# Performance work log

Hardware: AMD Instinct MI355X
Metric: run time of the kernel (lower is better)

The kernel has to match this reference:

```python
import jax, jax.numpy as jnp
import numpy as np

DIM = 1024
HEADS = 16
DIM_HEAD = 64
INNER = HEADS * DIM_HEAD  # 1024
EPS = 1e-5


def layer_norm(x, g, b):
    mu = jnp.mean(x, axis=-1, keepdims=True)
    var = jnp.var(x, axis=-1, keepdims=True)
    return (x - mu) * jax.lax.rsqrt(var + EPS) * g + b


def setup_inputs() -> dict:
    key = jax.random.key(0)
    ks = jax.random.split(key, 8)
    s = 0.02
    return {
        "x": jax.random.normal(ks[0], (2, 2048, DIM), dtype=jnp.float32),
        "w_qkv": jax.random.normal(ks[1], (DIM, 3 * INNER), dtype=jnp.float32) * s,
        "w_out": jax.random.normal(ks[2], (INNER, DIM), dtype=jnp.float32) * s,
        "b_out": jnp.zeros((DIM,), jnp.float32),
        "g1": jnp.ones((DIM,), jnp.float32),
        "bt1": jnp.zeros((DIM,), jnp.float32),
        "g2": jnp.ones((DIM,), jnp.float32),
        "bt2": jnp.zeros((DIM,), jnp.float32),
        "w1": jax.random.normal(ks[3], (DIM, DIM), dtype=jnp.float32) * s,  # ff hidden = dim_out = DIM
        "b1": jnp.zeros((DIM,), jnp.float32),
        "w2": jax.random.normal(ks[4], (DIM, DIM), dtype=jnp.float32) * s,
        "b2": jnp.zeros((DIM,), jnp.float32),
    }


def reference(x, w_qkv, w_out, b_out, g1, bt1, g2, bt2, w1, b1, w2, b2):
    b, n, _ = x.shape
    scale = DIM_HEAD ** (-0.5)
    x_in = x
    xl = layer_norm(x, g1, bt1)
    qkv = xl @ w_qkv  # [b, n, 3*inner]
    q, k, v = jnp.split(qkv, 3, axis=-1)
    def split_heads(t):
        return t.reshape(b, n, HEADS, DIM_HEAD).transpose(0, 2, 1, 3)  # b h n d
    q, k, v = map(split_heads, (q, k, v))
    dots = jnp.einsum('bhid,bhjd->bhij', q, k) * scale
    attn = jax.nn.softmax(dots, axis=-1)
    out = jnp.einsum('bhij,bhjd->bhid', attn, v)
    out = out.transpose(0, 2, 1, 3).reshape(b, n, INNER)
    out = out @ w_out + b_out
    out = out + x_in
    h = layer_norm(out, g2, bt2)
    h = jax.nn.gelu(h @ w1 + b1, approximate=False) @ w2 + b2
    return h + out
```

## Files before the change

kernel.cpp:

```cpp
#include <hip/hip_runtime.h>
#include <math.h>

typedef __attribute__((ext_vector_type(4))) float f32x4;
typedef __attribute__((ext_vector_type(8))) short bf16x8;
typedef __attribute__((ext_vector_type(8))) unsigned short u16x8;

#define DIM 1024
#define SEQ 2048
#define NHEADS 16
#define DH 64

__device__ __forceinline__ unsigned short f2bf(float f) {
    unsigned int u = __builtin_bit_cast(unsigned int, f);
    u += 0x7fffu + ((u >> 16) & 1u);
    return (unsigned short)(u >> 16);
}

__device__ __forceinline__ unsigned int cvt_pk_bf16(float lo, float hi) {
    unsigned int r;
    asm("v_cvt_pk_bf16_f32 %0, %1, %2" : "=v"(r) : "v"(lo), "v"(hi));
    return r;
}

__device__ __forceinline__ float fexp2(float x) {
    float r;
    asm("v_exp_f32 %0, %1" : "=v"(r) : "v"(x));
    return r;
}

__device__ __forceinline__ void gld16(const unsigned short* g, unsigned short* l) {
    __builtin_amdgcn_global_load_lds((const __attribute__((address_space(1))) void*)g,
                                     (__attribute__((address_space(3))) void*)l, 16, 0, 0);
}

__global__ __launch_bounds__(256) void wtrans_all(const float* __restrict__ wq,
                                                  const float* __restrict__ wo,
                                                  const float* __restrict__ wf1,
                                                  const float* __restrict__ wf2,
                                                  unsigned short* __restrict__ oq,
                                                  unsigned short* __restrict__ oo,
                                                  unsigned short* __restrict__ of1,
                                                  unsigned short* __restrict__ of2, float sc) {
    int z = blockIdx.z;
    int bxi = blockIdx.x;
    if (z > 0 && bxi >= 32) return;
    const float* w = z == 0 ? wq : z == 1 ? wo : z == 2 ? wf1 : wf2;
    unsigned short* wt = z == 0 ? oq : z == 1 ? oo : z == 2 ? of1 : of2;
    int N = z == 0 ? 3072 : 1024;
    int scale_n = z == 0 ? 1024 : 0;
    const int K = 1024;
    __shared__ float t[32][33];
    int tid = threadIdx.x;
    int n0 = bxi * 32, k0 = blockIdx.y * 32;
    int c = tid & 31, rb = tid >> 5;
#pragma unroll
    for (int i = 0; i < 4; ++i) {
        int r = rb + i * 8;
        t[r][c] = w[(size_t)(k0 + r) * N + n0 + c];
    }
    __syncthreads();
#pragma unroll
    for (int i = 0; i < 4; ++i) {
        int r = rb + i * 8;
        float v = t[c][r];
        if (n0 + r < scale_n) v *= sc;
        wt[(size_t)(n0 + r) * K + k0 + c] = f2bf(v);
    }
}

__global__ __launch_bounds__(256) void ln_kernel(const float* __restrict__ x,
                                                 const float* __restrict__ g,
                                                 const float* __restrict__ bt,
                                                 unsigned short* __restrict__ o) {
    int row = blockIdx.x, tid = threadIdx.x;
    const float4* xr = (const float4*)(x + (size_t)row * DIM);
    float4 v = xr[tid];
    float s1 = v.x + v.y + v.z + v.w;
    float s2 = v.x * v.x + v.y * v.y + v.z * v.z + v.w * v.w;
#pragma unroll
    for (int m = 32; m >= 1; m >>= 1) {
        s1 += __shfl_xor(s1, m);
        s2 += __shfl_xor(s2, m);
    }
    __shared__ float r1[4], r2[4];
    int w = tid >> 6;
    if ((tid & 63) == 0) { r1[w] = s1; r2[w] = s2; }
    __syncthreads();
    s1 = r1[0] + r1[1] + r1[2] + r1[3];
    s2 = r2[0] + r2[1] + r2[2] + r2[3];
    float mu = s1 * (1.0f / DIM);
    float var = s2 * (1.0f / DIM) - mu * mu;
    float rstd = rsqrtf(var + 1e-5f);
    float4 g4 = ((const float4*)g)[tid];
    float4 b4 = ((const float4*)bt)[tid];
    ushort4 ov;
    ov.x = f2bf((v.x - mu) * rstd * g4.x + b4.x);
    ov.y = f2bf((v.y - mu) * rstd * g4.y + b4.y);
    ov.z = f2bf((v.z - mu) * rstd * g4.z + b4.z);
    ov.w = f2bf((v.w - mu) * rstd * g4.w + b4.w);
    *(ushort4*)(o + (size_t)row * DIM + tid * 4) = ov;
}

template <int BN, int BK, int OBF, int BIAS, int GELU_, int RESID>
__global__ __launch_bounds__(256) void gemm_kernel(const unsigned short* __restrict__ A,
                                                   const unsigned short* __restrict__ BT,
                                                   void* __restrict__ C,
                                                   const float* __restrict__ bias,
                                                   const float* __restrict__ resid,
                                                   int M, int N, int K, int nbx) {
    constexpr int U = BK / 8;
    constexpr int NAU = 128 * U;
    constexpr int NBU = BN * U;
    constexpr int PT = (NAU + NBU) / 256;
    constexpr int NJ = BN / 32;
    constexpr int KK = BK / 32;
    __shared__ unsigned short As[3][128 * BK];
    __shared__ unsigned short Bs[3][BN * BK];
    int tid = threadIdx.x;
    int lane = tid & 63, w = tid >> 6;
    int l15 = lane & 15, lhi = lane >> 4;
    int nwg = gridDim.x, wg = blockIdx.x;
    int swz = (wg & 7) * (nwg >> 3) + (wg >> 3);
    int bx = swz % nbx, by = swz / nbx;
    int row0 = by * 128, col0 = bx * BN;
    int wrow = (w >> 1) * 64, wcol = (w & 1) * (16 * NJ);
    f32x4 zero = {0.f, 0.f, 0.f, 0.f};
    f32x4 acc[4][NJ];
#pragma unroll
    for (int i = 0; i < 4; ++i)
#pragma unroll
        for (int j = 0; j < NJ; ++j) acc[i][j] = zero;
    auto stage = [&](int buf, int kt) {
#pragma unroll
        for (int p = 0; p < PT; ++p) {
            if (p * 256 < NAU) {
                int u = tid + p * 256;
                int r = u / U, cu = u % U;
                int scu = cu ^ (r & (U - 1));
                gld16(A + (size_t)(row0 + r) * K + kt * BK + scu * 8, &As[buf][0] + u * 8);
            } else {
                int ub = tid + p * 256 - NAU;
                int r = ub / U, cu = ub % U;
                int scu = cu ^ (r & (U - 1));
                gld16(BT + (size_t)(col0 + r) * K + kt * BK + scu * 8, &Bs[buf][0] + ub * 8);
            }
        }
    };
    int nk = K / BK;
    stage(0, 0);
    stage(1, 1);
    asm volatile("s_waitcnt vmcnt(%0)" ::"i"(PT) : "memory");
    __builtin_amdgcn_s_barrier();
    __builtin_amdgcn_sched_barrier(0);
    int cur = 0;
    for (int kt = 0; kt < nk; ++kt) {
        int nxt2 = cur + 2 >= 3 ? cur - 1 : cur + 2;
        if (kt + 2 < nk) stage(nxt2, kt + 2);
        const unsigned short* Ab = &As[cur][0];
        const unsigned short* Bb = &Bs[cur][0];
        bf16x8 af[4][KK], bfr[NJ][KK];
#pragma unroll
        for (int i = 0; i < 4; ++i)
#pragma unroll
            for (int kk = 0; kk < KK; ++kk) {
                int rr = wrow + i * 16 + l15;
                int up = (kk * 4 + lhi) ^ (rr & (U - 1));
                af[i][kk] = *(const bf16x8*)&Ab[rr * BK + up * 8];
            }
#pragma unroll
        for (int j = 0; j < NJ; ++j)
#pragma unroll
            for (int kk = 0; kk < KK; ++kk) {
                int rr = wcol + j * 16 + l15;
                int up = (kk * 4 + lhi) ^ (rr & (U - 1));
                bfr[j][kk] = *(const bf16x8*)&Bb[rr * BK + up * 8];
            }
#pragma unroll
        for (int kk = 0; kk < KK; ++kk)
#pragma unroll
            for (int i = 0; i < 4; ++i)
#pragma unroll
                for (int j = 0; j < NJ; ++j)
                    acc[i][j] = __builtin_amdgcn_mfma_f32_16x16x32_bf16(af[i][kk], bfr[j][kk],
                                                                        acc[i][j], 0, 0, 0);
        __builtin_amdgcn_sched_barrier(0);
        if (kt + 1 < nk) {
            if (kt + 2 < nk)
                asm volatile("s_waitcnt vmcnt(%0)" ::"i"(PT) : "memory");
            else
                asm volatile("s_waitcnt vmcnt(0)" ::: "memory");
            __builtin_amdgcn_s_barrier();
            __builtin_amdgcn_sched_barrier(0);
        }
        cur = cur + 1 == 3 ? 0 : cur + 1;
    }
#pragma unroll
    for (int i = 0; i < 4; ++i)
#pragma unroll
        for (int j = 0; j < NJ; ++j)
#pragma unroll
            for (int r = 0; r < 4; ++r) {
                int row = row0 + wrow + i * 16 + lhi * 4 + r;
                int col = col0 + wcol + j * 16 + l15;
                float v = acc[i][j][r];
                if (BIAS) v += bias[col];
                if (GELU_) v = 0.5f * v * (1.0f + erff(v * 0.70710678118f));
                if (RESID) v += resid[(size_t)row * N + col];
                if (OBF)
                    ((unsigned short*)C)[(size_t)row * N + col] = f2bf(v);
                else
                    ((float*)C)[(size_t)row * N + col] = v;
            }
}

__global__ __launch_bounds__(256) void vtrans_kernel(const unsigned short* __restrict__ qkv,
                                                     unsigned short* __restrict__ vt) {
    __shared__ unsigned short t[64 * 72];
    int tid = threadIdx.x;
    int nt = blockIdx.x & 31, h = (blockIdx.x >> 5) & 15, b = blockIdx.x >> 9;
#pragma unroll
    for (int p = 0; p < 2; ++p) {
        int c = tid + p * 256;
        int n = c >> 3, s = (c & 7) * 8;
        *(uint4*)&t[n * 72 + s] =
            *(const uint4*)(qkv + (size_t)(b * SEQ + nt * 64 + n) * 3072 + 2048 + h * 64 + s);
    }
    __syncthreads();
#pragma unroll
    for (int p = 0; p < 2; ++p) {
        int c = tid + p * 256;
        int d = c >> 3, s0 = (c & 7) * 8;
        u16x8 val;
#pragma unroll
        for (int j = 0; j < 8; ++j) {
            int s = s0 + j;
            int sig = (s & 32) | ((s & 4) << 2) | ((s & 24) >> 1) | (s & 3);
            val[j] = t[sig * 72 + d];
        }
        *(u16x8*)(vt + ((size_t)(b * NHEADS + h) * DH + d) * SEQ + nt * 64 + s0) = val;
    }
}

__global__ __launch_bounds__(256) void attn_kernel(const unsigned short* __restrict__ qkv,
                                                   const unsigned short* __restrict__ vt,
                                                   unsigned short* __restrict__ o) {
    __shared__ unsigned short Ks[2][64 * 64];
    __shared__ unsigned short Vs[2][64 * 64];
    int tid = threadIdx.x;
    int lane = tid & 63, w = tid >> 6;
    int l15 = lane & 15, lhi = lane >> 4;
    int wg = blockIdx.x;
    int swz = (wg & 7) * 128 + (wg >> 3);
    int qt = swz & 31, h = (swz >> 5) & 15, b = swz >> 9;
    const unsigned short* qb =
        qkv + (size_t)(b * SEQ + qt * 64 + w * 16 + l15) * 3072 + h * DH;
    bf16x8 qf0 = *(const bf16x8*)(qb + lhi * 8);
    bf16x8 qf1 = *(const bf16x8*)(qb + 32 + lhi * 8);
    f32x4 zero = {0.f, 0.f, 0.f, 0.f};
    f32x4 oacc[4], lacc = zero;
#pragma unroll
    for (int i = 0; i < 4; ++i) oacc[i] = zero;
    const short one_s = (short)0x3F80;
    bf16x8 ones = {one_s, one_s, one_s, one_s, one_s, one_s, one_s, one_s};
    int srow = tid >> 3;
    int scx = (tid & 7) ^ (srow & 7);
    const unsigned short* kb = qkv + (size_t)b * SEQ * 3072 + 1024 + h * DH;
    const unsigned short* vb = vt + (size_t)(b * NHEADS + h) * DH * SEQ;
    const unsigned short* k0 = kb + (size_t)srow * 3072 + scx * 8;
    const unsigned short* v0 = vb + (size_t)srow * SEQ + scx * 8;
    auto stage = [&](int buf, int kt) {
        unsigned short* lk = &Ks[buf][0] + tid * 8;
        unsigned short* lv = &Vs[buf][0] + tid * 8;
        gld16(k0 + (size_t)kt * 64 * 3072, lk);
        gld16(k0 + ((size_t)kt * 64 + 32) * 3072, lk + 2048);
        gld16(v0 + kt * 64, lv);
        gld16(v0 + (size_t)32 * SEQ + kt * 64, lv + 2048);
    };
    const int NT = SEQ / 64;
    stage(0, 0);
    asm volatile("s_waitcnt vmcnt(0)" ::: "memory");
    __builtin_amdgcn_s_barrier();
    __builtin_amdgcn_sched_barrier(0);
    int kx = l15 & 7;
    for (int kt = 0; kt < NT; ++kt) {
        int cur = kt & 1;
        if (kt + 1 < NT) stage(cur ^ 1, kt + 1);
        const unsigned short* Kc = &Ks[cur][0];
        const unsigned short* Vc = &Vs[cur][0];
        f32x4 sacc[4];
#pragma unroll
        for (int nt = 0; nt < 4; ++nt) {
            bf16x8 kf0 = *(const bf16x8*)&Kc[(nt * 16 + l15) * 64 + ((lhi ^ kx) * 8)];
            bf16x8 kf1 = *(const bf16x8*)&Kc[(nt * 16 + l15) * 64 + (((4 + lhi) ^ kx) * 8)];
            f32x4 z = __builtin_amdgcn_mfma_f32_16x16x32_bf16(kf0, qf0, zero, 0, 0, 0);
            sacc[nt] = __builtin_amdgcn_mfma_f32_16x16x32_bf16(kf1, qf1, z, 0, 0, 0);
        }
        bf16x8 pf[2];
#pragma unroll
        for (int kc = 0; kc < 2; ++kc) {
            union { bf16x8 v; unsigned int u[4]; } pu;
            pu.u[0] = cvt_pk_bf16(fexp2(sacc[2 * kc][0]), fexp2(sacc[2 * kc][1]));
            pu.u[1] = cvt_pk_bf16(fexp2(sacc[2 * kc][2]), fexp2(sacc[2 * kc][3]));
            pu.u[2] = cvt_pk_bf16(fexp2(sacc[2 * kc + 1][0]), fexp2(sacc[2 * kc + 1][1]));
            pu.u[3] = cvt_pk_bf16(fexp2(sacc[2 * kc + 1][2]), fexp2(sacc[2 * kc + 1][3]));
            pf[kc] = pu.v;
        }
#pragma unroll
        for (int dt = 0; dt < 4; ++dt)
#pragma unroll
            for (int kc = 0; kc < 2; ++kc) {
                bf16x8 vf = *(const bf16x8*)&Vc[(dt * 16 + l15) * 64 + (((kc * 4 + lhi) ^ kx) * 8)];
                oacc[dt] = __builtin_amdgcn_mfma_f32_16x16x32_bf16(vf, pf[kc], oacc[dt], 0, 0, 0);
            }
        lacc = __builtin_amdgcn_mfma_f32_16x16x32_bf16(ones, pf[0], lacc, 0, 0, 0);
        lacc = __builtin_amdgcn_mfma_f32_16x16x32_bf16(ones, pf[1], lacc, 0, 0, 0);
        __builtin_amdgcn_sched_barrier(0);
        if (kt + 1 < NT) {
            asm volatile("s_waitcnt vmcnt(0)" ::: "memory");
            __builtin_amdgcn_s_barrier();
            __builtin_amdgcn_sched_barrier(0);
        }
    }
    float rl = 1.0f / lacc[0];
    size_t orow = (size_t)(b * SEQ + qt * 64 + w * 16 + l15) * DIM + h * DH;
#pragma unroll
    for (int dt = 0; dt < 4; ++dt) {
        ushort4 st;
        st.x = f2bf(oacc[dt][0] * rl);
        st.y = f2bf(oacc[dt][1] * rl);
        st.z = f2bf(oacc[dt][2] * rl);
        st.w = f2bf(oacc[dt][3] * rl);
        *(ushort4*)(o + orow + dt * 16 + lhi * 4) = st;
    }
}

extern "C" void kernel_launch(void* const* d_in, const int* in_sizes, int n_in,
                              void* d_out, int out_size, void* d_ws, size_t ws_size,
                              hipStream_t stream) {
    (void)in_sizes; (void)n_in; (void)out_size; (void)ws_size;
    const float* x = (const float*)d_in[0];
    const float* w_qkv = (const float*)d_in[1];
    const float* w_out = (const float*)d_in[2];
    const float* b_out = (const float*)d_in[3];
    const float* g1 = (const float*)d_in[4];
    const float* bt1 = (const float*)d_in[5];
    const float* g2 = (const float*)d_in[6];
    const float* bt2 = (const float*)d_in[7];
    const float* w1 = (const float*)d_in[8];
    const float* b1 = (const float*)d_in[9];
    const float* w2 = (const float*)d_in[10];
    const float* b2 = (const float*)d_in[11];
    float* out = (float*)d_out;

    char* ws = (char*)d_ws;
    size_t off = 0;
    auto alloc = [&](size_t bytes) {
        void* p = ws + off;
        off += (bytes + 255) & ~(size_t)255;
        return p;
    };
    const int R = 2 * SEQ;
    unsigned short* xl    = (unsigned short*)alloc((size_t)R * DIM * 2);
    unsigned short* wqkvT = (unsigned short*)alloc((size_t)3 * DIM * DIM * 2);
    unsigned short* woutT = (unsigned short*)alloc((size_t)DIM * DIM * 2);
    unsigned short* w1T   = (unsigned short*)alloc((size_t)DIM * DIM * 2);
    unsigned short* w2T   = (unsigned short*)alloc((size_t)DIM * DIM * 2);
    unsigned short* qkvb  = (unsigned short*)alloc((size_t)R * 3 * DIM * 2);
    unsigned short* vtb   = (unsigned short*)alloc((size_t)R * DIM * 2);
    unsigned short* attO  = (unsigned short*)alloc((size_t)R * DIM * 2);
    unsigned short* h2    = (unsigned short*)alloc((size_t)R * DIM * 2);
    unsigned short* ffn1  = (unsigned short*)alloc((size_t)R * DIM * 2);

    const float CS = 0.125f * 1.44269504f;
    wtrans_all<<<dim3(96, 32, 4), 256, 0, stream>>>(w_qkv, w_out, w1, w2, wqkvT, woutT, w1T, w2T, CS);

    ln_kernel<<<R, 256, 0, stream>>>(x, g1, bt1, xl);
    gemm_kernel<128, 32, 1, 0, 0, 0><<<dim3((3 * DIM / 128) * (R / 128)), 256, 0, stream>>>(
        xl, wqkvT, qkvb, nullptr, nullptr, R, 3 * DIM, DIM, 3 * DIM / 128);
    vtrans_kernel<<<2 * NHEADS * (SEQ / 64), 256, 0, stream>>>(qkvb, vtb);
    attn_kernel<<<2 * NHEADS * (SEQ / 64), 256, 0, stream>>>(qkvb, vtb, attO);
    gemm_kernel<64, 64, 0, 1, 0, 1><<<dim3((DIM / 64) * (R / 128)), 256, 0, stream>>>(
        attO, woutT, out, b_out, x, R, DIM, DIM, DIM / 64);
    ln_kernel<<<R, 256, 0, stream>>>(out, g2, bt2, h2);
    gemm_kernel<64, 64, 1, 1, 1, 0><<<dim3((DIM / 64) * (R / 128)), 256, 0, stream>>>(
        h2, w1T, ffn1, b1, nullptr, R, DIM, DIM, DIM / 64);
    gemm_kernel<64, 64, 0, 1, 0, 1><<<dim3((DIM / 64) * (R / 128)), 256, 0, stream>>>(
        ffn1, w2T, out, b2, out, R, DIM, DIM, DIM / 64);
}
```

Before: 168.4 us.

## Split attention over two KV halves and combine partials in a new kernel

```diff
diff --git a/kernel.cpp b/kernel.cpp
--- a/kernel.cpp
+++ b/kernel.cpp
@@ -243,15 +243,16 @@
 
 __global__ __launch_bounds__(256) void attn_kernel(const unsigned short* __restrict__ qkv,
                                                    const unsigned short* __restrict__ vt,
-                                                   unsigned short* __restrict__ o) {
-    __shared__ unsigned short Ks[2][64 * 64];
-    __shared__ unsigned short Vs[2][64 * 64];
+                                                   float* __restrict__ po,
+                                                   float* __restrict__ pl) {
+    __shared__ unsigned short Ks[64 * 64];
+    __shared__ unsigned short Vs[64 * 64];
     int tid = threadIdx.x;
     int lane = tid & 63, w = tid >> 6;
     int l15 = lane & 15, lhi = lane >> 4;
     int wg = blockIdx.x;
-    int swz = (wg & 7) * 128 + (wg >> 3);
-    int qt = swz & 31, h = (swz >> 5) & 15, b = swz >> 9;
+    int swz = (wg & 7) * 256 + (wg >> 3);
+    int qt = swz & 31, half = (swz >> 5) & 1, h = (swz >> 6) & 15, b = swz >> 10;
     const unsigned short* qb =
         qkv + (size_t)(b * SEQ + qt * 64 + w * 16 + l15) * 3072 + h * DH;
     bf16x8 qf0 = *(const bf16x8*)(qb + lhi * 8);
@@ -268,30 +269,26 @@
     const unsigned short* vb = vt + (size_t)(b * NHEADS + h) * DH * SEQ;
     const unsigned short* k0 = kb + (size_t)srow * 3072 + scx * 8;
     const unsigned short* v0 = vb + (size_t)srow * SEQ + scx * 8;
-    auto stage = [&](int buf, int kt) {
-        unsigned short* lk = &Ks[buf][0] + tid * 8;
-        unsigned short* lv = &Vs[buf][0] + tid * 8;
-        gld16(k0 + (size_t)kt * 64 * 3072, lk);
-        gld16(k0 + ((size_t)kt * 64 + 32) * 3072, lk + 2048);
-        gld16(v0 + kt * 64, lv);
-        gld16(v0 + (size_t)32 * SEQ + kt * 64, lv + 2048);
+    auto stage = [&](int kg) {
+        unsigned short* lk = &Ks[0] + tid * 8;
+        unsigned short* lv = &Vs[0] + tid * 8;
+        gld16(k0 + (size_t)kg * 64 * 3072, lk);
+        gld16(k0 + ((size_t)kg * 64 + 32) * 3072, lk + 2048);
+        gld16(v0 + kg * 64, lv);
+        gld16(v0 + (size_t)32 * SEQ + kg * 64, lv + 2048);
     };
-    const int NT = SEQ / 64;
-    stage(0, 0);
-    asm volatile("s_waitcnt vmcnt(0)" ::: "memory");
-    __builtin_amdgcn_s_barrier();
-    __builtin_amdgcn_sched_barrier(0);
     int kx = l15 & 7;
-    for (int kt = 0; kt < NT; ++kt) {
-        int cur = kt & 1;
-        if (kt + 1 < NT) stage(cur ^ 1, kt + 1);
-        const unsigned short* Kc = &Ks[cur][0];
-        const unsigned short* Vc = &Vs[cur][0];
+    const int NT2 = SEQ / 64 / 2;
+    for (int kt = 0; kt < NT2; ++kt) {
+        stage(half * NT2 + kt);
+        asm volatile("s_waitcnt vmcnt(0)" ::: "memory");
+        __builtin_amdgcn_s_barrier();
+        __builtin_amdgcn_sched_barrier(0);
         f32x4 sacc[4];
 #pragma unroll
         for (int nt = 0; nt < 4; ++nt) {
-            bf16x8 kf0 = *(const bf16x8*)&Kc[(nt * 16 + l15) * 64 + ((lhi ^ kx) * 8)];
-            bf16x8 kf1 = *(const bf16x8*)&Kc[(nt * 16 + l15) * 64 + (((4 + lhi) ^ kx) * 8)];
+            bf16x8 kf0 = *(const bf16x8*)&Ks[(nt * 16 + l15) * 64 + ((lhi ^ kx) * 8)];
+            bf16x8 kf1 = *(const bf16x8*)&Ks[(nt * 16 + l15) * 64 + (((4 + lhi) ^ kx) * 8)];
             f32x4 z = __builtin_amdgcn_mfma_f32_16x16x32_bf16(kf0, qf0, zero, 0, 0, 0);
             sacc[nt] = __builtin_amdgcn_mfma_f32_16x16x32_bf16(kf1, qf1, z, 0, 0, 0);
         }
@@ -309,29 +306,41 @@
         for (int dt = 0; dt < 4; ++dt)
 #pragma unroll
             for (int kc = 0; kc < 2; ++kc) {
-                bf16x8 vf = *(const bf16x8*)&Vc[(dt * 16 + l15) * 64 + (((kc * 4 + lhi) ^ kx) * 8)];
+                bf16x8 vf = *(const bf16x8*)&Vs[(dt * 16 + l15) * 64 + (((kc * 4 + lhi) ^ kx) * 8)];
                 oacc[dt] = __builtin_amdgcn_mfma_f32_16x16x32_bf16(vf, pf[kc], oacc[dt], 0, 0, 0);
             }
         lacc = __builtin_amdgcn_mfma_f32_16x16x32_bf16(ones, pf[0], lacc, 0, 0, 0);
         lacc = __builtin_amdgcn_mfma_f32_16x16x32_bf16(ones, pf[1], lacc, 0, 0, 0);
         __builtin_amdgcn_sched_barrier(0);
-        if (kt + 1 < NT) {
-            asm volatile("s_waitcnt vmcnt(0)" ::: "memory");
+        if (kt + 1 < NT2) {
             __builtin_amdgcn_s_barrier();
             __builtin_amdgcn_sched_barrier(0);
         }
     }
-    float rl = 1.0f / lacc[0];
-    size_t orow = (size_t)(b * SEQ + qt * 64 + w * 16 + l15) * DIM + h * DH;
+    int rrow = b * SEQ + qt * 64 + w * 16 + l15;
+    float* pob = po + ((size_t)half * 4096 + rrow) * DIM + h * DH;
 #pragma unroll
     for (int dt = 0; dt < 4; ++dt) {
-        ushort4 st;
-        st.x = f2bf(oacc[dt][0] * rl);
-        st.y = f2bf(oacc[dt][1] * rl);
-        st.z = f2bf(oacc[dt][2] * rl);
-        st.w = f2bf(oacc[dt][3] * rl);
-        *(ushort4*)(o + orow + dt * 16 + lhi * 4) = st;
-    }
+        float4 st = {oacc[dt][0], oacc[dt][1], oacc[dt][2], oacc[dt][3]};
+        *(float4*)(pob + dt * 16 + lhi * 4) = st;
+    }
+    if (lhi == 0) pl[((size_t)half * 4096 + rrow) * NHEADS + h] = lacc[0];
+}
+
+__global__ __launch_bounds__(256) void attn_combine(const float* __restrict__ po,
+                                                    const float* __restrict__ pl,
+                                                    unsigned short* __restrict__ o) {
+    int r = blockIdx.x, tid = threadIdx.x;
+    int d0 = tid * 4, h = d0 >> 6;
+    float4 a = *(const float4*)(po + (size_t)r * DIM + d0);
+    float4 c = *(const float4*)(po + (size_t)(4096 + r) * DIM + d0);
+    float rl = 1.0f / (pl[(size_t)r * NHEADS + h] + pl[(size_t)(4096 + r) * NHEADS + h]);
+    ushort4 ov;
+    ov.x = f2bf((a.x + c.x) * rl);
+    ov.y = f2bf((a.y + c.y) * rl);
+    ov.z = f2bf((a.z + c.z) * rl);
+    ov.w = f2bf((a.w + c.w) * rl);
+    *(ushort4*)(o + (size_t)r * DIM + d0) = ov;
 }
 
 extern "C" void kernel_launch(void* const* d_in, const int* in_sizes, int n_in,
@@ -370,6 +379,8 @@
     unsigned short* attO  = (unsigned short*)alloc((size_t)R * DIM * 2);
     unsigned short* h2    = (unsigned short*)alloc((size_t)R * DIM * 2);
     unsigned short* ffn1  = (unsigned short*)alloc((size_t)R * DIM * 2);
+    float* po = (float*)alloc((size_t)2 * R * DIM * 4);
+    float* pl = (float*)alloc((size_t)2 * R * NHEADS * 4);
 
     const float CS = 0.125f * 1.44269504f;
     wtrans_all<<<dim3(96, 32, 4), 256, 0, stream>>>(w_qkv, w_out, w1, w2, wqkvT, woutT, w1T, w2T, CS);
@@ -378,7 +389,8 @@
     gemm_kernel<128, 32, 1, 0, 0, 0><<<dim3((3 * DIM / 128) * (R / 128)), 256, 0, stream>>>(
         xl, wqkvT, qkvb, nullptr, nullptr, R, 3 * DIM, DIM, 3 * DIM / 128);
     vtrans_kernel<<<2 * NHEADS * (SEQ / 64), 256, 0, stream>>>(qkvb, vtb);
-    attn_kernel<<<2 * NHEADS * (SEQ / 64), 256, 0, stream>>>(qkvb, vtb, attO);
+    attn_kernel<<<2 * NHEADS * (SEQ / 64) * 2, 256, 0, stream>>>(qkvb, vtb, po, pl);
+    attn_combine<<<R, 256, 0, stream>>>(po, pl, attO);
     gemm_kernel<64, 64, 0, 1, 0, 1><<<dim3((DIM / 64) * (R / 128)), 256, 0, stream>>>(
         attO, woutT, out, b_out, x, R, DIM, DIM, DIM / 64);
     ln_kernel<<<R, 256, 0, stream>>>(out, g2, bt2, h2);
```

Result: slower. 178.8 us (+6.2%).

## Fuse LN1 into weight transpose, V-transpose into QKV GEMM, store residual in bf16

Applied to the files above, without the earlier changes.

```diff
diff --git a/kernel.cpp b/kernel.cpp
--- a/kernel.cpp
+++ b/kernel.cpp
@@ -16,6 +16,11 @@
     return (unsigned short)(u >> 16);
 }
 
+__device__ __forceinline__ float bf2f(unsigned short s) {
+    unsigned int u = (unsigned int)s << 16;
+    return __builtin_bit_cast(float, u);
+}
+
 __device__ __forceinline__ unsigned int cvt_pk_bf16(float lo, float hi) {
     unsigned int r;
     asm("v_cvt_pk_bf16_f32 %0, %1, %2" : "=v"(r) : "v"(lo), "v"(hi));
@@ -33,24 +38,58 @@
                                      (__attribute__((address_space(3))) void*)l, 16, 0, 0);
 }
 
-__global__ __launch_bounds__(256) void wtrans_all(const float* __restrict__ wq,
-                                                  const float* __restrict__ wo,
-                                                  const float* __restrict__ wf1,
-                                                  const float* __restrict__ wf2,
-                                                  unsigned short* __restrict__ oq,
-                                                  unsigned short* __restrict__ oo,
-                                                  unsigned short* __restrict__ of1,
-                                                  unsigned short* __restrict__ of2, float sc) {
+__global__ __launch_bounds__(256) void wtrans_ln(const float* __restrict__ wq,
+                                                 const float* __restrict__ wo,
+                                                 const float* __restrict__ wf1,
+                                                 const float* __restrict__ wf2,
+                                                 unsigned short* __restrict__ oq,
+                                                 unsigned short* __restrict__ oo,
+                                                 unsigned short* __restrict__ of1,
+                                                 unsigned short* __restrict__ of2, float sc,
+                                                 const float* __restrict__ x,
+                                                 const float* __restrict__ g1,
+                                                 const float* __restrict__ bt1,
+                                                 unsigned short* __restrict__ xl) {
     int z = blockIdx.z;
     int bxi = blockIdx.x;
-    if (z > 0 && bxi >= 32) return;
+    int tid = threadIdx.x;
+    if (z == 4) {
+        int row = blockIdx.y * 128 + bxi;
+        const float4* xr = (const float4*)(x + (size_t)row * DIM);
+        float4 v = xr[tid];
+        float s1 = v.x + v.y + v.z + v.w;
+        float s2 = v.x * v.x + v.y * v.y + v.z * v.z + v.w * v.w;
+#pragma unroll
+        for (int m = 32; m >= 1; m >>= 1) {
+            s1 += __shfl_xor(s1, m);
+            s2 += __shfl_xor(s2, m);
+        }
+        __shared__ float r1[4], r2[4];
+        int w = tid >> 6;
+        if ((tid & 63) == 0) { r1[w] = s1; r2[w] = s2; }
+        __syncthreads();
+        s1 = r1[0] + r1[1] + r1[2] + r1[3];
+        s2 = r2[0] + r2[1] + r2[2] + r2[3];
+        float mu = s1 * (1.0f / DIM);
+        float var = s2 * (1.0f / DIM) - mu * mu;
+        float rstd = rsqrtf(var + 1e-5f);
+        float4 g4 = ((const float4*)g1)[tid];
+        float4 b4 = ((const float4*)bt1)[tid];
+        ushort4 ov;
+        ov.x = f2bf((v.x - mu) * rstd * g4.x + b4.x);
+        ov.y = f2bf((v.y - mu) * rstd * g4.y + b4.y);
+        ov.z = f2bf((v.z - mu) * rstd * g4.z + b4.z);
+        ov.w = f2bf((v.w - mu) * rstd * g4.w + b4.w);
+        *(ushort4*)(xl + (size_t)row * DIM + tid * 4) = ov;
+        return;
+    }
+    if (bxi >= (z == 0 ? 96 : 32)) return;
     const float* w = z == 0 ? wq : z == 1 ? wo : z == 2 ? wf1 : wf2;
     unsigned short* wt = z == 0 ? oq : z == 1 ? oo : z == 2 ? of1 : of2;
     int N = z == 0 ? 3072 : 1024;
     int scale_n = z == 0 ? 1024 : 0;
     const int K = 1024;
     __shared__ float t[32][33];
-    int tid = threadIdx.x;
     int n0 = bxi * 32, k0 = blockIdx.y * 32;
     int c = tid & 31, rb = tid >> 5;
 #pragma unroll
@@ -68,15 +107,15 @@
     }
 }
 
-__global__ __launch_bounds__(256) void ln_kernel(const float* __restrict__ x,
-                                                 const float* __restrict__ g,
-                                                 const float* __restrict__ bt,
-                                                 unsigned short* __restrict__ o) {
+__global__ __launch_bounds__(256) void ln_bf16(const unsigned short* __restrict__ x,
+                                               const float* __restrict__ g,
+                                               const float* __restrict__ bt,
+                                               unsigned short* __restrict__ o) {
     int row = blockIdx.x, tid = threadIdx.x;
-    const float4* xr = (const float4*)(x + (size_t)row * DIM);
-    float4 v = xr[tid];
-    float s1 = v.x + v.y + v.z + v.w;
-    float s2 = v.x * v.x + v.y * v.y + v.z * v.z + v.w * v.w;
+    ushort4 v4 = *(const ushort4*)(x + (size_t)row * DIM + tid * 4);
+    float vx = bf2f(v4.x), vy = bf2f(v4.y), vz = bf2f(v4.z), vw = bf2f(v4.w);
+    float s1 = vx + vy + vz + vw;
+    float s2 = vx * vx + vy * vy + vz * vz + vw * vw;
 #pragma unroll
     for (int m = 32; m >= 1; m >>= 1) {
         s1 += __shfl_xor(s1, m);
@@ -94,19 +133,20 @@
     float4 g4 = ((const float4*)g)[tid];
     float4 b4 = ((const float4*)bt)[tid];
     ushort4 ov;
-    ov.x = f2bf((v.x - mu) * rstd * g4.x + b4.x);
-    ov.y = f2bf((v.y - mu) * rstd * g4.y + b4.y);
-    ov.z = f2bf((v.z - mu) * rstd * g4.z + b4.z);
-    ov.w = f2bf((v.w - mu) * rstd * g4.w + b4.w);
+    ov.x = f2bf((vx - mu) * rstd * g4.x + b4.x);
+    ov.y = f2bf((vy - mu) * rstd * g4.y + b4.y);
+    ov.z = f2bf((vz - mu) * rstd * g4.z + b4.z);
+    ov.w = f2bf((vw - mu) * rstd * g4.w + b4.w);
     *(ushort4*)(o + (size_t)row * DIM + tid * 4) = ov;
 }
 
-template <int BN, int BK, int OBF, int BIAS, int GELU_, int RESID>
+template <int BN, int BK, int OBF, int BIAS, int GELU_, int RESID, int VT>
 __global__ __launch_bounds__(256) void gemm_kernel(const unsigned short* __restrict__ A,
                                                    const unsigned short* __restrict__ BT,
                                                    void* __restrict__ C,
                                                    const float* __restrict__ bias,
-                                                   const float* __restrict__ resid,
+                                                   const void* __restrict__ resid,
+                                                   unsigned short* __restrict__ vt,
                                                    int M, int N, int K, int nbx) {
     constexpr int U = BK / 8;
     constexpr int NAU = 128 * U;
@@ -114,8 +154,9 @@
     constexpr int PT = (NAU + NBU) / 256;
     constexpr int NJ = BN / 32;
     constexpr int KK = BK / 32;
-    __shared__ unsigned short As[3][128 * BK];
-    __shared__ unsigned short Bs[3][BN * BK];
+    extern __shared__ char smem[];
+    unsigned short* As = (unsigned short*)smem;
+    unsigned short* Bs = As + 3 * 128 * BK;
     int tid = threadIdx.x;
     int lane = tid & 63, w = tid >> 6;
     int l15 = lane & 15, lhi = lane >> 4;
@@ -137,12 +178,12 @@
                 int u = tid + p * 256;
                 int r = u / U, cu = u % U;
                 int scu = cu ^ (r & (U - 1));
-                gld16(A + (size_t)(row0 + r) * K + kt * BK + scu * 8, &As[buf][0] + u * 8);
+                gld16(A + (size_t)(row0 + r) * K + kt * BK + scu * 8, As + buf * 128 * BK + u * 8);
             } else {
                 int ub = tid + p * 256 - NAU;
                 int r = ub / U, cu = ub % U;
                 int scu = cu ^ (r & (U - 1));
-                gld16(BT + (size_t)(col0 + r) * K + kt * BK + scu * 8, &Bs[buf][0] + ub * 8);
+                gld16(BT + (size_t)(col0 + r) * K + kt * BK + scu * 8, Bs + buf * BN * BK + ub * 8);
             }
         }
     };
@@ -156,8 +197,8 @@
     for (int kt = 0; kt < nk; ++kt) {
         int nxt2 = cur + 2 >= 3 ? cur - 1 : cur + 2;
         if (kt + 2 < nk) stage(nxt2, kt + 2);
-        const unsigned short* Ab = &As[cur][0];
-        const unsigned short* Bb = &Bs[cur][0];
+        const unsigned short* Ab = As + cur * 128 * BK;
+        const unsigned short* Bb = Bs + cur * BN * BK;
         bf16x8 af[4][KK], bfr[NJ][KK];
 #pragma unroll
         for (int i = 0; i < 4; ++i)
@@ -194,6 +235,29 @@
         }
         cur = cur + 1 == 3 ? 0 : cur + 1;
     }
+    if (VT && col0 >= 2048) {
+        __syncthreads();
+        unsigned short* Ct = (unsigned short*)smem;
+#pragma unroll
+        for (int i = 0; i < 4; ++i)
+#pragma unroll
+            for (int j = 0; j < NJ; ++j)
+#pragma unroll
+                for (int r = 0; r < 4; ++r)
+                    Ct[(wrow + i * 16 + lhi * 4 + r) * 130 + (wcol + j * 16 + l15)] =
+                        f2bf(acc[i][j][r]);
+        __syncthreads();
+        int l = tid & 63, wv = tid >> 6;
+        int sig = (l & 32) | ((l & 4) << 2) | ((l & 24) >> 1) | (l & 3);
+        int b = row0 >> 11, n0 = row0 & 2047;
+        int h0 = (col0 - 2048) >> 6;
+        for (int c = wv * 64; c < wv * 64 + 64; ++c) {
+            int ntl = c & 1, hl = (c >> 1) & 1, d = c >> 2;
+            unsigned short v = Ct[(ntl * 64 + sig) * 130 + hl * 64 + d];
+            vt[((size_t)(b * NHEADS + h0 + hl) * DH + d) * SEQ + n0 + ntl * 64 + l] = v;
+        }
+        return;
+    }
 #pragma unroll
     for (int i = 0; i < 4; ++i)
 #pragma unroll
@@ -205,40 +269,13 @@
                 float v = acc[i][j][r];
                 if (BIAS) v += bias[col];
                 if (GELU_) v = 0.5f * v * (1.0f + erff(v * 0.70710678118f));
-                if (RESID) v += resid[(size_t)row * N + col];
+                if (RESID == 1) v += ((const float*)resid)[(size_t)row * N + col];
+                if (RESID == 2) v += bf2f(((const unsigned short*)resid)[(size_t)row * N + col]);
                 if (OBF)
                     ((unsigned short*)C)[(size_t)row * N + col] = f2bf(v);
                 else
                     ((float*)C)[(size_t)row * N + col] = v;
             }
-}
-
-__global__ __launch_bounds__(256) void vtrans_kernel(const unsigned short* __restrict__ qkv,
-                                                     unsigned short* __restrict__ vt) {
-    __shared__ unsigned short t[64 * 72];
-    int tid = threadIdx.x;
-    int nt = blockIdx.x & 31, h = (blockIdx.x >> 5) & 15, b = blockIdx.x >> 9;
-#pragma unroll
-    for (int p = 0; p < 2; ++p) {
-        int c = tid + p * 256;
-        int n = c >> 3, s = (c & 7) * 8;
-        *(uint4*)&t[n * 72 + s] =
-            *(const uint4*)(qkv + (size_t)(b * SEQ + nt * 64 + n) * 3072 + 2048 + h * 64 + s);
-    }
-    __syncthreads();
-#pragma unroll
-    for (int p = 0; p < 2; ++p) {
-        int c = tid + p * 256;
-        int d = c >> 3, s0 = (c & 7) * 8;
-        u16x8 val;
-#pragma unroll
-        for (int j = 0; j < 8; ++j) {
-            int s = s0 + j;
-            int sig = (s & 32) | ((s & 4) << 2) | ((s & 24) >> 1) | (s & 3);
-            val[j] = t[sig * 72 + d];
-        }
-        *(u16x8*)(vt + ((size_t)(b * NHEADS + h) * DH + d) * SEQ + nt * 64 + s0) = val;
-    }
 }
 
 __global__ __launch_bounds__(256) void attn_kernel(const unsigned short* __restrict__ qkv,
@@ -368,22 +405,25 @@
     unsigned short* qkvb  = (unsigned short*)alloc((size_t)R * 3 * DIM * 2);
     unsigned short* vtb   = (unsigned short*)alloc((size_t)R * DIM * 2);
     unsigned short* attO  = (unsigned short*)alloc((size_t)R * DIM * 2);
+    unsigned short* outb  = (unsigned short*)alloc((size_t)R * DIM * 2);
     unsigned short* h2    = (unsigned short*)alloc((size_t)R * DIM * 2);
     unsigned short* ffn1  = (unsigned short*)alloc((size_t)R * DIM * 2);
 
     const float CS = 0.125f * 1.44269504f;
-    wtrans_all<<<dim3(96, 32, 4), 256, 0, stream>>>(w_qkv, w_out, w1, w2, wqkvT, woutT, w1T, w2T, CS);
-
-    ln_kernel<<<R, 256, 0, stream>>>(x, g1, bt1, xl);
-    gemm_kernel<128, 32, 1, 0, 0, 0><<<dim3((3 * DIM / 128) * (R / 128)), 256, 0, stream>>>(
-        xl, wqkvT, qkvb, nullptr, nullptr, R, 3 * DIM, DIM, 3 * DIM / 128);
-    vtrans_kernel<<<2 * NHEADS * (SEQ / 64), 256, 0, stream>>>(qkvb, vtb);
+    wtrans_ln<<<dim3(128, 32, 5), 256, 0, stream>>>(w_qkv, w_out, w1, w2, wqkvT, woutT, w1T, w2T,
+                                                    CS, x, g1, bt1, xl);
+
+    const unsigned int SH_QKV = (3 * 128 * 32 + 3 * 128 * 32) * 2;
+    const unsigned int SH_FFN = (3 * 128 * 64 + 3 * 64 * 64) * 2;
+    gemm_kernel<128, 32, 1, 0, 0, 0, 1>
+        <<<dim3((3 * DIM / 128) * (R / 128)), 256, SH_QKV, stream>>>(
+            xl, wqkvT, qkvb, nullptr, nullptr, vtb, R, 3 * DIM, DIM, 3 * DIM / 128);
     attn_kernel<<<2 * NHEADS * (SEQ / 64), 256, 0, stream>>>(qkvb, vtb, attO);
-    gemm_kernel<64, 64, 0, 1, 0, 1><<<dim3((DIM / 64) * (R / 128)), 256, 0, stream>>>(
-        attO, woutT, out, b_out, x, R, DIM, DIM, DIM / 64);
-    ln_kernel<<<R, 256, 0, stream>>>(out, g2, bt2, h2);
-    gemm_kernel<64, 64, 1, 1, 1, 0><<<dim3((DIM / 64) * (R / 128)), 256, 0, stream>>>(
-        h2, w1T, ffn1, b1, nullptr, R, DIM, DIM, DIM / 64);
-    gemm_kernel<64, 64, 0, 1, 0, 1><<<dim3((DIM / 64) * (R / 128)), 256, 0, stream>>>(
-        ffn1, w2T, out, b2, out, R, DIM, DIM, DIM / 64);
-}
+    gemm_kernel<64, 64, 1, 1, 0, 1, 0><<<dim3((DIM / 64) * (R / 128)), 256, SH_FFN, stream>>>(
+        attO, woutT, outb, b_out, x, nullptr, R, DIM, DIM, DIM / 64);
+    ln_bf16<<<R, 256, 0, stream>>>(outb, g2, bt2, h2);
+    gemm_kernel<64, 64, 1, 1, 1, 0, 0><<<dim3((DIM / 64) * (R / 128)), 256, SH_FFN, stream>>>(
+        h2, w1T, ffn1, b1, nullptr, nullptr, R, DIM, DIM, DIM / 64);
+    gemm_kernel<64, 64, 0, 1, 0, 2, 0><<<dim3((DIM / 64) * (R / 128)), 256, SH_FFN, stream>>>(
+        ffn1, w2T, out, b2, outb, nullptr, R, DIM, DIM, DIM / 64);
+}
```

Result: faster. 160.3 us (-4.8%).
